# Performance work log

Measured on AMD Instinct MI355X. Metric: run time of the kernel, lower is better.

## Reference

```python
import jax, jax.numpy as jnp
import numpy as np

DIM = 1536
N_HEADS = 12
HEAD_DIM = DIM // N_HEADS  # 128
EPS = 1e-6
B, L = 2, 2048


def _rms_norm(x, g, eps=EPS):
    # WanRMSNorm: normalize in fp32 over last dim, scale by g
    xf = x.astype(jnp.float32)
    y = xf * jax.lax.rsqrt(jnp.mean(xf * xf, axis=-1, keepdims=True) + eps)
    return (y * g).astype(x.dtype)


def _apply_rotary(x, freqs):
    # x: [b, s, n, d]; freqs: [1, s, 2d] -> cos/sin each [1, s, 1, d]
    cos, sin = jnp.split(freqs[:, :, None, :], 2, axis=-1)
    b, s, n, d = x.shape
    xr = x.reshape(b, s, n, d // 2, 2)
    rot = jnp.stack([-xr[..., 1], xr[..., 0]], axis=-1).reshape(b, s, n, d)
    out = x.astype(jnp.float32) * cos + rot.astype(jnp.float32) * sin
    return out.astype(x.dtype)


def setup_inputs() -> dict:
    key = jax.random.key(0)
    ks = jax.random.split(key, 12)
    scale = 1.0 / np.sqrt(DIM)
    x = jax.random.normal(ks[0], (B, L, DIM), dtype=jnp.float32)
    wq = jax.random.normal(ks[1], (DIM, DIM), dtype=jnp.float32) * scale
    bq = jnp.zeros((DIM,), dtype=jnp.float32)
    wk = jax.random.normal(ks[2], (DIM, DIM), dtype=jnp.float32) * scale
    bk = jnp.zeros((DIM,), dtype=jnp.float32)
    wv = jax.random.normal(ks[3], (DIM, DIM), dtype=jnp.float32) * scale
    bv = jnp.zeros((DIM,), dtype=jnp.float32)
    wo = jax.random.normal(ks[4], (DIM, DIM), dtype=jnp.float32) * scale
    bo = jnp.zeros((DIM,), dtype=jnp.float32)
    gq = jnp.ones((DIM,), dtype=jnp.float32)
    gk = jnp.ones((DIM,), dtype=jnp.float32)
    # real RoPE table: interleaved-pair cos/sin, concatenated -> [1, L, 2*HEAD_DIM]
    half = HEAD_DIM // 2
    inv_freq = 1.0 / (10000.0 ** (np.arange(half, dtype=np.float32) / half))
    ang = np.arange(L, dtype=np.float32)[:, None] * inv_freq[None, :]  # [L, half]
    cos = np.repeat(np.cos(ang), 2, axis=-1)  # [L, HEAD_DIM]
    sin = np.repeat(np.sin(ang), 2, axis=-1)
    freqs = jnp.asarray(np.concatenate([cos, sin], axis=-1)[None])  # [1, L, 2*HEAD_DIM]
    seq_lens = jnp.array([L, 3 * L // 4], dtype=jnp.int32)
    grid_sizes = jnp.array([[16, 16, 8], [16, 12, 8]], dtype=jnp.int32)
    return {"x": x, "wq": wq, "bq": bq, "wk": wk, "bk": bk, "wv": wv, "bv": bv,
            "wo": wo, "bo": bo, "gq": gq, "gk": gk, "freqs": freqs,
            "seq_lens": seq_lens, "grid_sizes": grid_sizes}


def reference(x, wq, bq, wk, bk, wv, bv, wo, bo, gq, gk, freqs, seq_lens, grid_sizes):
    b, s, _ = x.shape
    n, d = N_HEADS, HEAD_DIM
    q = _rms_norm(x @ wq.T + bq, gq).reshape(b, s, n, d)
    k = _rms_norm(x @ wk.T + bk, gk).reshape(b, s, n, d)
    v = (x @ wv.T + bv).reshape(b, s, n, d)
    q = _apply_rotary(q, freqs)
    k = _apply_rotary(k, freqs)
    # variable-length attention: mask keys j >= seq_lens[b]; window (-1,-1) = full
    scores = jnp.einsum("bqnd,bknd->bnqk", q, k) * (1.0 / np.sqrt(d))
    key_mask = (jnp.arange(s)[None, :] < seq_lens[:, None])[:, None, None, :]  # [b,1,1,s]
    scores = jnp.where(key_mask, scores, jnp.finfo(scores.dtype).min)
    probs = jax.nn.softmax(scores, axis=-1)
    out = jnp.einsum("bnqk,bknd->bqnd", probs, v).reshape(b, s, n * d)
    return out @ wo.T + bo
```

## Files before the change

### kernel.cpp

```cpp
#include <hip/hip_runtime.h>
#include <stdint.h>

typedef unsigned short u16;
typedef __bf16 bfx8 __attribute__((ext_vector_type(8)));
typedef short  sx4  __attribute__((ext_vector_type(4)));
typedef float  fx4  __attribute__((ext_vector_type(4)));
typedef u16    ux8  __attribute__((ext_vector_type(8)));
typedef u16    ux4  __attribute__((ext_vector_type(4)));
typedef float  flt4 __attribute__((ext_vector_type(4)));

#define DIM   1536
#define NH    12
#define HD    128
#define BATCH 2
#define SEQ   2048
#define MTOK  (BATCH*SEQ)
#define EPSV  1e-6f
#define SCALE 0.08838834764831845f
#define NX    (MTOK*DIM)
#define NW    (DIM*DIM)

__device__ __forceinline__ u16 f2bf(float x){
  union { float f; uint32_t u; } v; v.f = x;
  return (u16)((v.u + 0x7FFFu + ((v.u >> 16) & 1u)) >> 16);
}
__device__ __forceinline__ float bf2f(u16 h){
  union { uint32_t u; float f; } v; v.u = ((uint32_t)h) << 16; return v.f;
}
__device__ __forceinline__ void gl_lds16(const void* g, void* l){
  __builtin_amdgcn_global_load_lds((const __attribute__((address_space(1))) void*)g,
                                   (__attribute__((address_space(3))) void*)l, 16, 0, 0);
}
__device__ __forceinline__ fx4 fzero(){ fx4 z = {0.f,0.f,0.f,0.f}; return z; }

__global__ __launch_bounds__(256)
void convert_k(const float* __restrict__ x, const float* __restrict__ wq,
               const float* __restrict__ wk, const float* __restrict__ wv,
               const float* __restrict__ wo,
               u16* __restrict__ xb, u16* __restrict__ wqb, u16* __restrict__ wkb,
               u16* __restrict__ wvb, u16* __restrict__ wob)
{
  const long i4 = (long)(blockIdx.x * 256 + threadIdx.x) * 4;
  const float* src; u16* dst; long off;
  if (i4 < NX){ src = x; dst = xb; off = i4; }
  else {
    long j = i4 - NX;
    if      (j < (long)NW)   { src = wq; dst = wqb; off = j; }
    else if (j < 2L*NW)      { src = wk; dst = wkb; off = j - NW; }
    else if (j < 3L*NW)      { src = wv; dst = wvb; off = j - 2L*NW; }
    else                     { src = wo; dst = wob; off = j - 3L*NW; }
  }
  flt4 v = *(const flt4*)(src + off);
  ux4 o;
  o[0] = f2bf(v[0]); o[1] = f2bf(v[1]); o[2] = f2bf(v[2]); o[3] = f2bf(v[3]);
  *(ux4*)(dst + off) = o;
}

#define BM 128
#define BN 128
#define BK 64

template<int MODE>
__device__ __forceinline__ void gemm_core(u16* sA, u16* sB,
                                          const u16* __restrict__ A, const u16* __restrict__ W,
                                          const float* __restrict__ bias,
                                          u16* __restrict__ outb, float* __restrict__ outf,
                                          float* __restrict__ sumsq)
{
  const int t = threadIdx.x;
  const int lane = t & 63;
  const int wid = t >> 6;
  const int wm = wid >> 1, wn = wid & 1;
  const int quad = lane >> 4, l15 = lane & 15;
  const int m0 = blockIdx.y * BM;
  const int n0 = blockIdx.x * BN;

  fx4 acc[4][4];
  #pragma unroll
  for (int i = 0; i < 4; ++i)
    #pragma unroll
    for (int j = 0; j < 4; ++j) acc[i][j] = fzero();

  const int ri  = t >> 3;
  const int sg0 = t & 7;

  for (int kb = 0; kb < DIM/BK; ++kb){
    const int k0 = kb * BK;
    #pragma unroll
    for (int s = 0; s < 4; ++s){
      const int row = s*32 + ri;
      const int sa = sg0 ^ (row & 7);
      gl_lds16(A + (m0+row)*DIM + k0 + sa*8, (char*)sA + s*4096 + t*16);
      gl_lds16(W + (n0+row)*DIM + k0 + sa*8, (char*)sB + s*4096 + t*16);
    }
    __syncthreads();
    #pragma unroll
    for (int kk = 0; kk < 2; ++kk){
      bfx8 af[4], bw[4];
      #pragma unroll
      for (int i = 0; i < 4; ++i){
        const int rA = wm*64 + i*16 + l15;
        af[i] = *(const bfx8*)((const char*)sA + rA*128 + (((kk*4 + quad) ^ (rA & 7)) * 16));
        const int rB = wn*64 + i*16 + l15;
        bw[i] = *(const bfx8*)((const char*)sB + rB*128 + (((kk*4 + quad) ^ (rB & 7)) * 16));
      }
      #pragma unroll
      for (int i = 0; i < 4; ++i)
        #pragma unroll
        for (int j = 0; j < 4; ++j)
          acc[i][j] = __builtin_amdgcn_mfma_f32_16x16x32_bf16(af[i], bw[j], acc[i][j], 0, 0, 0);
    }
    __syncthreads();
  }

  float bvals[4];
  #pragma unroll
  for (int j = 0; j < 4; ++j) bvals[j] = bias[n0 + wn*64 + j*16 + l15];

  #pragma unroll
  for (int i = 0; i < 4; ++i){
    #pragma unroll
    for (int r = 0; r < 4; ++r){
      const int grow = m0 + wm*64 + i*16 + quad*4 + r;
      float s2 = 0.f;
      #pragma unroll
      for (int j = 0; j < 4; ++j){
        const int gcol = n0 + wn*64 + j*16 + l15;
        const float v = acc[i][j][r] + bvals[j];
        if (MODE == 2) outf[grow*DIM + gcol] = v;
        else           outb[grow*DIM + gcol] = f2bf(v);
        s2 += v*v;
      }
      if (MODE == 0){
        s2 += __shfl_xor(s2, 1);
        s2 += __shfl_xor(s2, 2);
        s2 += __shfl_xor(s2, 4);
        s2 += __shfl_xor(s2, 8);
        if (l15 == 0) atomicAdd(&sumsq[grow], s2);
      }
    }
  }
}

__global__ __launch_bounds__(256)
void gemm_qkv_k(const u16* __restrict__ xb,
                const u16* __restrict__ wqb, const u16* __restrict__ wkb, const u16* __restrict__ wvb,
                const float* __restrict__ bq, const float* __restrict__ bk, const float* __restrict__ bv,
                u16* __restrict__ qraw, u16* __restrict__ kraw, u16* __restrict__ vraw,
                float* __restrict__ ssq, float* __restrict__ ssk)
{
  __shared__ u16 sA[BM*BK];
  __shared__ u16 sB[BN*BK];
  const int z = blockIdx.z;
  if (z == 0)      gemm_core<0>(sA, sB, xb, wqb, bq, qraw, nullptr, ssq);
  else if (z == 1) gemm_core<0>(sA, sB, xb, wkb, bk, kraw, nullptr, ssk);
  else             gemm_core<1>(sA, sB, xb, wvb, bv, vraw, nullptr, nullptr);
}

__global__ __launch_bounds__(256)
void gemm_out_k(const u16* __restrict__ attnb, const u16* __restrict__ wob,
                const float* __restrict__ bo, float* __restrict__ out)
{
  __shared__ u16 sA[BM*BK];
  __shared__ u16 sB[BN*BK];
  gemm_core<2>(sA, sB, attnb, wob, bo, nullptr, out, nullptr);
}

__global__ __launch_bounds__(256)
void normrope_k(const u16* __restrict__ qraw, const u16* __restrict__ kraw,
                const float* __restrict__ ssq, const float* __restrict__ ssk,
                const float* __restrict__ gq, const float* __restrict__ gk,
                const float* __restrict__ freqs,
                u16* __restrict__ qbf, u16* __restrict__ kbf)
{
  const int row = blockIdx.x;
  const int isK = blockIdx.y;
  const u16* src   = isK ? kraw : qraw;
  const float* ss  = isK ? ssk  : ssq;
  const float* g   = isK ? gk   : gq;
  u16* dst         = isK ? kbf  : qbf;
  const int spos = row & (SEQ - 1);
  const float rstd = rsqrtf(ss[row] * (1.0f/DIM) + EPSV);
  #pragma unroll
  for (int it = 0; it < 3; ++it){
    const int p = threadIdx.x + it*256;
    const int d = p*2;
    const int hd = d & (HD-1);
    const uint32_t two = *(const uint32_t*)(src + row*DIM + d);
    const float y0 = bf2f((u16)(two & 0xFFFFu)) * rstd * g[d];
    const float y1 = bf2f((u16)(two >> 16))     * rstd * g[d+1];
    const float c  = freqs[spos*(2*HD) + hd];
    const float sn = freqs[spos*(2*HD) + HD + hd];
    const float o0 = y0*c - y1*sn;
    const float o1 = y1*c + y0*sn;
    *(uint32_t*)(dst + row*DIM + d) = (uint32_t)f2bf(o0) | ((uint32_t)f2bf(o1) << 16);
  }
}

__global__ __launch_bounds__(256)
void transpose_v_k(const u16* __restrict__ v, u16* __restrict__ vt)
{
  __shared__ u16 tile[64][65];
  const int t  = threadIdx.x;
  const int b  = blockIdx.z;
  const int t0 = blockIdx.x * 64;
  const int g0 = blockIdx.y * 64;
  const int r8 = t >> 3;
  const int c8 = (t & 7) * 8;
  #pragma unroll
  for (int i = 0; i < 2; ++i){
    const int row = i*32 + r8;
    ux8 val = *(const ux8*)(v + (b*SEQ + t0 + row)*DIM + g0 + c8);
    #pragma unroll
    for (int j = 0; j < 8; ++j) tile[c8 + j][row] = val[j];
  }
  __syncthreads();
  #pragma unroll
  for (int i = 0; i < 2; ++i){
    const int drow = i*32 + r8;
    const int dg = g0 + drow;
    const int h = dg >> 7, dd = dg & (HD-1);
    ux8 o;
    #pragma unroll
    for (int j = 0; j < 8; ++j) o[j] = tile[drow][c8 + j];
    *(ux8*)(vt + ((b*NH + h)*HD + dd)*SEQ + t0 + c8) = o;
  }
}

__global__ __launch_bounds__(256)
void flash_k(const u16* __restrict__ qbf, const u16* __restrict__ kbf, const u16* __restrict__ vt,
             const int* __restrict__ seq_lens, u16* __restrict__ attnb)
{
  __shared__ char smem[49152];
  const int t = threadIdx.x;
  const int lane = t & 63, w = t >> 6;
  const int quad = lane >> 4, l15 = lane & 15;
  const int qt = blockIdx.x, h = blockIdx.y, b = blockIdx.z;
  const int q0 = qt * 64;
  const int tokbase = b * SEQ;
  const int kvlen = min(seq_lens[b], SEQ);
  const int ntiles = (kvlen + 63) >> 6;

  {
    const int ri = t >> 4, seg = t & 15;
    #pragma unroll
    for (int s = 0; s < 4; ++s){
      const int row = s*16 + ri;
      const int sg = seg ^ (row & 15);
      gl_lds16(qbf + (tokbase + q0 + row)*DIM + h*HD + sg*8, smem + s*4096 + t*16);
    }
  }

  fx4 o[8];
  #pragma unroll
  for (int i = 0; i < 8; ++i) o[i] = fzero();
  float mrow = -1e30f, lrow = 0.f;

  for (int kt = 0; kt < ntiles; ++kt){
    {
      const int ri = t >> 4, seg = t & 15;
      #pragma unroll
      for (int s = 0; s < 4; ++s){
        const int row = s*16 + ri;
        const int sg = seg ^ (row & 15);
        gl_lds16(kbf + (tokbase + kt*64 + row)*DIM + h*HD + sg*8, smem + 16384 + s*4096 + t*16);
      }
    }
    {
      const int ri = t >> 3, seg = t & 7;
      #pragma unroll
      for (int s = 0; s < 4; ++s){
        const int row = s*32 + ri;
        const int sg = seg ^ (row & 7);
        gl_lds16(vt + ((b*NH + h)*HD + row)*SEQ + kt*64 + sg*8, smem + 32768 + s*4096 + t*16);
      }
    }
    __syncthreads();

    fx4 st[4];
    #pragma unroll
    for (int i = 0; i < 4; ++i) st[i] = fzero();
    #pragma unroll
    for (int kk = 0; kk < 4; ++kk){
      const int qrow = w*16 + l15;
      const bfx8 qf = *(const bfx8*)(smem + qrow*256 + (((kk*4 + quad) ^ (qrow & 15)) * 16));
      #pragma unroll
      for (int i = 0; i < 4; ++i){
        const int krow = i*16 + l15;
        const bfx8 kf = *(const bfx8*)(smem + 16384 + krow*256 + (((kk*4 + quad) ^ (krow & 15)) * 16));
        st[i] = __builtin_amdgcn_mfma_f32_16x16x32_bf16(kf, qf, st[i], 0, 0, 0);
      }
    }

    float sc[4][4];
    float tm = -1e30f;
    #pragma unroll
    for (int i = 0; i < 4; ++i){
      #pragma unroll
      for (int r = 0; r < 4; ++r){
        float vv = st[i][r] * SCALE;
        const int key = kt*64 + i*16 + quad*4 + r;
        if (key >= kvlen) vv = -1e30f;
        sc[i][r] = vv;
        tm = fmaxf(tm, vv);
      }
    }
    tm = fmaxf(tm, __shfl_xor(tm, 16));
    tm = fmaxf(tm, __shfl_xor(tm, 32));
    const float mnew  = fmaxf(mrow, tm);
    const float alpha = __expf(mrow - mnew);
    float ps = 0.f;
    sx4 pb[4];
    #pragma unroll
    for (int i = 0; i < 4; ++i){
      #pragma unroll
      for (int r = 0; r < 4; ++r){
        const float p = __expf(sc[i][r] - mnew);
        ps += p;
        pb[i][r] = (short)f2bf(p);
      }
    }
    ps += __shfl_xor(ps, 16);
    ps += __shfl_xor(ps, 32);
    lrow = lrow * alpha + ps;
    mrow = mnew;
    #pragma unroll
    for (int i = 0; i < 8; ++i){
      o[i][0] *= alpha; o[i][1] *= alpha; o[i][2] *= alpha; o[i][3] *= alpha;
    }

    #pragma unroll
    for (int ks = 0; ks < 4; ++ks){
      #pragma unroll
      for (int dt = 0; dt < 8; ++dt){
        const int dim = dt*16 + l15;
        const int sg = (2*ks + (quad >> 1)) ^ (dim & 7);
        const sx4 vf = *(const sx4*)(smem + 32768 + dim*128 + sg*16 + (quad & 1)*8);
        o[dt] = __builtin_amdgcn_mfma_f32_16x16x16bf16_1k(vf, pb[ks], o[dt], 0, 0, 0);
      }
    }
    __syncthreads();
  }

  const float inv = 1.0f / lrow;
  u16* Os = (u16*)smem;
  const int qrow = w*16 + l15;
  #pragma unroll
  for (int dt = 0; dt < 8; ++dt)
    #pragma unroll
    for (int r = 0; r < 4; ++r)
      Os[qrow*136 + dt*16 + quad*4 + r] = f2bf(o[dt][r] * inv);
  __syncthreads();
  {
    const int ri = t >> 4, seg = t & 15;
    #pragma unroll
    for (int s = 0; s < 4; ++s){
      const int row = s*16 + ri;
      const ux8 val = *(const ux8*)(Os + row*136 + seg*8);
      *(ux8*)(attnb + (tokbase + q0 + row)*DIM + h*HD + seg*8) = val;
    }
  }
}

extern "C" void kernel_launch(void* const* d_in, const int* in_sizes, int n_in,
                              void* d_out, int out_size, void* d_ws, size_t ws_size,
                              hipStream_t stream)
{
  (void)in_sizes; (void)n_in; (void)out_size; (void)ws_size;
  const float* x      = (const float*)d_in[0];
  const float* wq     = (const float*)d_in[1];
  const float* bq     = (const float*)d_in[2];
  const float* wk     = (const float*)d_in[3];
  const float* bk     = (const float*)d_in[4];
  const float* wv     = (const float*)d_in[5];
  const float* bv     = (const float*)d_in[6];
  const float* wo     = (const float*)d_in[7];
  const float* bo     = (const float*)d_in[8];
  const float* gq     = (const float*)d_in[9];
  const float* gk     = (const float*)d_in[10];
  const float* freqs  = (const float*)d_in[11];
  const int*   seqls  = (const int*)d_in[12];

  char* ws = (char*)d_ws;
  u16* xb   = (u16*)(ws + 0);
  u16* wqb  = (u16*)(ws + 12582912);
  u16* wkb  = (u16*)(ws + 17301504);
  u16* wvb  = (u16*)(ws + 22020096);
  u16* wob  = (u16*)(ws + 26738688);
  u16* qraw = (u16*)(ws + 31457280);
  u16* kraw = (u16*)(ws + 44040192);
  u16* vraw = (u16*)(ws + 56623104);
  u16* qbf  = (u16*)(ws + 69206016);
  u16* kbf  = (u16*)(ws + 81788928);
  float* ssq = (float*)(ws + 94371840);
  float* ssk = (float*)(ws + 94388224);
  u16* vt    = xb;
  u16* attnb = qraw;

  (void)hipMemsetAsync(ssq, 0, 32768, stream);

  convert_k   <<<15360, 256, 0, stream>>>(x, wq, wk, wv, wo, xb, wqb, wkb, wvb, wob);
  gemm_qkv_k  <<<dim3(12, 32, 3), 256, 0, stream>>>(xb, wqb, wkb, wvb, bq, bk, bv,
                                                    qraw, kraw, vraw, ssq, ssk);
  normrope_k  <<<dim3(4096, 2), 256, 0, stream>>>(qraw, kraw, ssq, ssk, gq, gk, freqs, qbf, kbf);
  transpose_v_k<<<dim3(32, 24, 2), 256, 0, stream>>>(vraw, vt);
  flash_k     <<<dim3(32, 12, 2), 256, 0, stream>>>(qbf, kbf, vt, seqls, attnb);
  gemm_out_k  <<<dim3(12, 32), 256, 0, stream>>>(attnb, wob, bo, (float*)d_out);
}
```

Before: 360.8 us.

## Rewrite flash attention with 32x32 MFMA, split-K waves and register-resident Q

```diff
diff --git a/kernel.cpp b/kernel.cpp
--- a/kernel.cpp
+++ b/kernel.cpp
@@ -5,6 +5,7 @@
 typedef __bf16 bfx8 __attribute__((ext_vector_type(8)));
 typedef short  sx4  __attribute__((ext_vector_type(4)));
 typedef float  fx4  __attribute__((ext_vector_type(4)));
+typedef float  fx16 __attribute__((ext_vector_type(16)));
 typedef u16    ux8  __attribute__((ext_vector_type(8)));
 typedef u16    ux4  __attribute__((ext_vector_type(4)));
 typedef float  flt4 __attribute__((ext_vector_type(4)));
@@ -180,7 +181,8 @@
   const float* g   = isK ? gk   : gq;
   u16* dst         = isK ? kbf  : qbf;
   const int spos = row & (SEQ - 1);
-  const float rstd = rsqrtf(ss[row] * (1.0f/DIM) + EPSV);
+  float rstd = rsqrtf(ss[row] * (1.0f/DIM) + EPSV);
+  if (!isK) rstd *= SCALE;
   #pragma unroll
   for (int it = 0; it < 3; ++it){
     const int p = threadIdx.x + it*256;
@@ -227,137 +229,179 @@
   }
 }
 
-__global__ __launch_bounds__(256)
+__global__ __launch_bounds__(256, 3)
 void flash_k(const u16* __restrict__ qbf, const u16* __restrict__ kbf, const u16* __restrict__ vt,
              const int* __restrict__ seq_lens, u16* __restrict__ attnb)
 {
   __shared__ char smem[49152];
   const int t = threadIdx.x;
-  const int lane = t & 63, w = t >> 6;
-  const int quad = lane >> 4, l15 = lane & 15;
-  const int qt = blockIdx.x, h = blockIdx.y, b = blockIdx.z;
-  const int q0 = qt * 64;
+  const int lane = t & 63;
+  const int h = lane >> 5;
+  const int l31 = lane & 31;
+  const int wq = (t >> 6) & 1;
+  const int wk = t >> 7;
+  const int hh = blockIdx.y, b = blockIdx.z;
+  const int q0 = blockIdx.x * 64 + wq * 32;
   const int tokbase = b * SEQ;
   const int kvlen = min(seq_lens[b], SEQ);
   const int ntiles = (kvlen + 63) >> 6;
 
+  bfx8 qf[8];
   {
-    const int ri = t >> 4, seg = t & 15;
-    #pragma unroll
-    for (int s = 0; s < 4; ++s){
-      const int row = s*16 + ri;
-      const int sg = seg ^ (row & 15);
-      gl_lds16(qbf + (tokbase + q0 + row)*DIM + h*HD + sg*8, smem + s*4096 + t*16);
-    }
-  }
-
-  fx4 o[8];
-  #pragma unroll
-  for (int i = 0; i < 8; ++i) o[i] = fzero();
+    const u16* qp = qbf + (size_t)(tokbase + q0 + l31)*DIM + hh*HD + h*8;
+    #pragma unroll
+    for (int c = 0; c < 8; ++c) qf[c] = *(const bfx8*)(qp + c*16);
+  }
+
+  fx16 o[4];
+  #pragma unroll
+  for (int dt = 0; dt < 4; ++dt)
+    #pragma unroll
+    for (int r = 0; r < 16; ++r) o[dt][r] = 0.f;
   float mrow = -1e30f, lrow = 0.f;
+
+  const int kri = t >> 4, kseg = t & 15;
+  const int vri = t >> 3, vseg = t & 7;
+  const int krow = wk*32 + l31;
 
   for (int kt = 0; kt < ntiles; ++kt){
     {
-      const int ri = t >> 4, seg = t & 15;
       #pragma unroll
       for (int s = 0; s < 4; ++s){
-        const int row = s*16 + ri;
-        const int sg = seg ^ (row & 15);
-        gl_lds16(kbf + (tokbase + kt*64 + row)*DIM + h*HD + sg*8, smem + 16384 + s*4096 + t*16);
+        const int row = s*16 + kri;
+        const int sg = kseg ^ (row & 15);
+        gl_lds16(kbf + (size_t)(tokbase + kt*64 + row)*DIM + hh*HD + sg*8, smem + s*4096 + t*16);
       }
     }
     {
-      const int ri = t >> 3, seg = t & 7;
       #pragma unroll
       for (int s = 0; s < 4; ++s){
-        const int row = s*32 + ri;
-        const int sg = seg ^ (row & 7);
-        gl_lds16(vt + ((b*NH + h)*HD + row)*SEQ + kt*64 + sg*8, smem + 32768 + s*4096 + t*16);
+        const int row = s*32 + vri;
+        const int sg = vseg ^ (row & 7);
+        gl_lds16(vt + (size_t)((b*NH + hh)*HD + row)*SEQ + kt*64 + sg*8, smem + 16384 + s*4096 + t*16);
       }
     }
     __syncthreads();
 
-    fx4 st[4];
-    #pragma unroll
-    for (int i = 0; i < 4; ++i) st[i] = fzero();
-    #pragma unroll
-    for (int kk = 0; kk < 4; ++kk){
-      const int qrow = w*16 + l15;
-      const bfx8 qf = *(const bfx8*)(smem + qrow*256 + (((kk*4 + quad) ^ (qrow & 15)) * 16));
-      #pragma unroll
-      for (int i = 0; i < 4; ++i){
-        const int krow = i*16 + l15;
-        const bfx8 kf = *(const bfx8*)(smem + 16384 + krow*256 + (((kk*4 + quad) ^ (krow & 15)) * 16));
-        st[i] = __builtin_amdgcn_mfma_f32_16x16x32_bf16(kf, qf, st[i], 0, 0, 0);
-      }
-    }
-
-    float sc[4][4];
-    float tm = -1e30f;
-    #pragma unroll
-    for (int i = 0; i < 4; ++i){
-      #pragma unroll
-      for (int r = 0; r < 4; ++r){
-        float vv = st[i][r] * SCALE;
-        const int key = kt*64 + i*16 + quad*4 + r;
-        if (key >= kvlen) vv = -1e30f;
-        sc[i][r] = vv;
-        tm = fmaxf(tm, vv);
-      }
-    }
-    tm = fmaxf(tm, __shfl_xor(tm, 16));
+    fx16 st;
+    #pragma unroll
+    for (int r = 0; r < 16; ++r) st[r] = 0.f;
+    #pragma unroll
+    for (int c = 0; c < 8; ++c){
+      const bfx8 kf = *(const bfx8*)(smem + krow*256 + (((2*c + h) ^ (krow & 15)) << 4));
+      st = __builtin_amdgcn_mfma_f32_32x32x16_bf16(kf, qf[c], st, 0, 0, 0);
+    }
+
+    if ((kt == ntiles - 1) && (kvlen & 63)){
+      #pragma unroll
+      for (int r = 0; r < 16; ++r){
+        const int key = kt*64 + wk*32 + (r & 3) + 8*(r >> 2) + 4*h;
+        if (key >= kvlen) st[r] = -1e30f;
+      }
+    }
+
+    float tm = st[0];
+    #pragma unroll
+    for (int r = 1; r < 16; ++r) tm = fmaxf(tm, st[r]);
     tm = fmaxf(tm, __shfl_xor(tm, 32));
-    const float mnew  = fmaxf(mrow, tm);
-    const float alpha = __expf(mrow - mnew);
+    if (__any(tm > mrow)){
+      const float mnew = fmaxf(mrow, tm);
+      const float alpha = __expf(mrow - mnew);
+      lrow *= alpha;
+      #pragma unroll
+      for (int dt = 0; dt < 4; ++dt)
+        #pragma unroll
+        for (int r = 0; r < 16; ++r) o[dt][r] *= alpha;
+      mrow = mnew;
+    }
+
+    uint32_t tt[16];
     float ps = 0.f;
+    #pragma unroll
+    for (int r = 0; r < 16; ++r){
+      union { float f; uint32_t u; } e; e.f = __expf(st[r] - mrow);
+      const uint32_t u = e.u + 0x8000u;
+      tt[r] = u;
+      union { uint32_t u; float f; } pm; pm.u = u & 0xFFFF0000u;
+      ps += pm.f;
+    }
+    ps += __shfl_xor(ps, 32);
+    lrow += ps;
+
     sx4 pb[4];
     #pragma unroll
-    for (int i = 0; i < 4; ++i){
-      #pragma unroll
-      for (int r = 0; r < 4; ++r){
-        const float p = __expf(sc[i][r] - mnew);
-        ps += p;
-        pb[i][r] = (short)f2bf(p);
-      }
-    }
-    ps += __shfl_xor(ps, 16);
-    ps += __shfl_xor(ps, 32);
-    lrow = lrow * alpha + ps;
-    mrow = mnew;
-    #pragma unroll
-    for (int i = 0; i < 8; ++i){
-      o[i][0] *= alpha; o[i][1] *= alpha; o[i][2] *= alpha; o[i][3] *= alpha;
-    }
-
-    #pragma unroll
     for (int ks = 0; ks < 4; ++ks){
-      #pragma unroll
-      for (int dt = 0; dt < 8; ++dt){
-        const int dim = dt*16 + l15;
-        const int sg = (2*ks + (quad >> 1)) ^ (dim & 7);
-        const sx4 vf = *(const sx4*)(smem + 32768 + dim*128 + sg*16 + (quad & 1)*8);
-        o[dt] = __builtin_amdgcn_mfma_f32_16x16x16bf16_1k(vf, pb[ks], o[dt], 0, 0, 0);
+      union { uint32_t u[2]; sx4 s; } pk;
+      pk.u[0] = __builtin_amdgcn_perm(tt[4*ks+1], tt[4*ks+0], 0x07060302u);
+      pk.u[1] = __builtin_amdgcn_perm(tt[4*ks+3], tt[4*ks+2], 0x07060302u);
+      pb[ks] = pk.s;
+    }
+
+    #pragma unroll
+    for (int ks = 0; ks < 4; ++ks){
+      #pragma unroll
+      for (int dt = 0; dt < 4; ++dt){
+        const int row = dt*32 + l31;
+        const sx4 vf = *(const sx4*)(smem + 16384 + row*128 + ((((wk<<2) + ks) ^ (row & 7)) << 4) + (h << 3));
+        o[dt] = __builtin_amdgcn_mfma_f32_32x32x8bf16_1k(vf, pb[ks], o[dt], 0, 0, 0);
       }
     }
     __syncthreads();
   }
 
-  const float inv = 1.0f / lrow;
-  u16* Os = (u16*)smem;
-  const int qrow = w*16 + l15;
-  #pragma unroll
-  for (int dt = 0; dt < 8; ++dt)
-    #pragma unroll
-    for (int r = 0; r < 4; ++r)
-      Os[qrow*136 + dt*16 + quad*4 + r] = f2bf(o[dt][r] * inv);
+  float* mlbuf = (float*)(smem + 32768);
+  if (h == 0){
+    mlbuf[((wk*2 + wq)*2 + 0)*32 + l31] = mrow;
+    mlbuf[((wk*2 + wq)*2 + 1)*32 + l31] = lrow;
+  }
+  __syncthreads();
+  const float mo = mlbuf[(((wk^1)*2 + wq)*2 + 0)*32 + l31];
+  const float lo = mlbuf[(((wk^1)*2 + wq)*2 + 1)*32 + l31];
+  const float M  = fmaxf(mrow, mo);
+  const float f  = __expf(mrow - M);
+  const float L  = lrow * f + lo * __expf(mo - M);
+  #pragma unroll
+  for (int dt = 0; dt < 4; ++dt)
+    #pragma unroll
+    for (int r = 0; r < 16; ++r) o[dt][r] *= f;
+  __syncthreads();
+
+  float* xbuf = (float*)smem;
+  if (wk == 1){
+    #pragma unroll
+    for (int dt = 0; dt < 4; ++dt)
+      #pragma unroll
+      for (int rq = 0; rq < 4; ++rq){
+        const int d = dt*32 + 8*rq + 4*h;
+        fx4 v4; v4[0]=o[dt][4*rq]; v4[1]=o[dt][4*rq+1]; v4[2]=o[dt][4*rq+2]; v4[3]=o[dt][4*rq+3];
+        *(fx4*)(xbuf + (size_t)(wq*32 + l31)*128 + d) = v4;
+      }
+  }
+  __syncthreads();
+
+  u16* Os = (u16*)(smem + 32768);
+  if (wk == 0){
+    const float invL = 1.0f / L;
+    #pragma unroll
+    for (int dt = 0; dt < 4; ++dt)
+      #pragma unroll
+      for (int rq = 0; rq < 4; ++rq){
+        const int d = dt*32 + 8*rq + 4*h;
+        const fx4 p4 = *(const fx4*)(xbuf + (size_t)(wq*32 + l31)*128 + d);
+        ux4 b4;
+        #pragma unroll
+        for (int j = 0; j < 4; ++j) b4[j] = f2bf((o[dt][4*rq + j] + p4[j]) * invL);
+        *(ux4*)(Os + (size_t)(wq*32 + l31)*128 + d) = b4;
+      }
+  }
   __syncthreads();
   {
     const int ri = t >> 4, seg = t & 15;
     #pragma unroll
     for (int s = 0; s < 4; ++s){
       const int row = s*16 + ri;
-      const ux8 val = *(const ux8*)(Os + row*136 + seg*8);
-      *(ux8*)(attnb + (tokbase + q0 + row)*DIM + h*HD + seg*8) = val;
+      const ux8 val = *(const ux8*)(Os + row*128 + seg*8);
+      *(ux8*)(attnb + (size_t)(tokbase + blockIdx.x*64 + row)*DIM + hh*HD + seg*8) = val;
     }
   }
 }
```

After: 344.6 us. 1.05x faster.
